# Performance work log

Hardware: AMD Instinct MI355X
Metric: run time of the kernel (lower is better)

## Reference

```python
import jax, jax.numpy as jnp
from jax import lax
import numpy as np

STRIDE = 4
RADIUS = 0.2
NSAMPLE = 32
DENSITY_K = 16
INTRINSIC_DIM = 3
EPS = 1e-8
BN_EPS = 1e-5


def _cdist(a, b):
    # Euclidean pairwise distances: a (..., M, 3), b (..., N, 3) -> (..., M, N)
    d2 = ((a * a).sum(-1)[..., :, None] + (b * b).sum(-1)[..., None, :]
          - 2.0 * jnp.matmul(a, jnp.swapaxes(b, -1, -2)))
    return jnp.sqrt(jnp.maximum(d2, 1e-12))


def _fps(coords, n_samples):
    # iterative farthest point sampling: coords (B, N, 3) -> (B, n_samples) int32
    B, N, _ = coords.shape
    mean = coords.mean(axis=1, keepdims=True)
    farthest = jnp.argmax(((coords - mean) ** 2).sum(-1), axis=1)
    min_dist = jnp.full((B, N), jnp.inf, dtype=coords.dtype)

    def step(carry, _):
        md, far = carry
        centroid = jnp.take_along_axis(coords, far[:, None, None], axis=1)  # (B,1,3)
        d = ((coords - centroid) ** 2).sum(-1)
        md = jnp.minimum(md, d)
        return (md, jnp.argmax(md, axis=1)), far

    _, idxs = lax.scan(step, (min_dist, farthest), None, length=n_samples)
    return idxs.T  # (B, n_samples)


def _ball_query(q, s, radius, k):
    d = _cdist(q, s)  # (B, M, N)
    _, knn_idx = lax.top_k(-d, k)                 # k nearest fallback
    masked = jnp.where(d > radius, jnp.inf, d)
    neg_vals, m_idx = lax.top_k(-masked, k)       # k nearest within radius
    valid = jnp.isfinite(neg_vals)
    return jnp.where(valid, m_idx, knn_idx)


def _density_weights(gc):
    # gc: (B, M, K, 3) -> weights (B, M, K); kth-NN-distance based density weights
    K = gc.shape[2]
    d = _cdist(gc, gc)  # (B, M, K, K)
    d = jnp.where(jnp.eye(K, dtype=bool), jnp.inf, d)
    kk = min(max(DENSITY_K, 1), K - 1)
    kth = -lax.top_k(-d, kk)[0][..., -1]  # distance to kk-th neighbor, (B, M, K)
    raw = jnp.maximum(kth, EPS) ** INTRINSIC_DIM
    return raw / jnp.maximum(raw.sum(axis=-1, keepdims=True), EPS)


def _bn(x, g, b, axes):
    # training-mode batchnorm (biased variance), channel axis = 1
    mu = x.mean(axes, keepdims=True)
    var = x.var(axes, keepdims=True)
    shp = [1] * x.ndim
    shp[1] = -1
    return (x - mu) / jnp.sqrt(var + BN_EPS) * g.reshape(shp) + b.reshape(shp)


def setup_inputs() -> dict:
    key = jax.random.key(0)
    ks = jax.random.split(key, 5)
    B, N, C_in, C_out = 8, 4096, 64, 128
    mid = C_out // 2  # stride > 1 -> mid_channels = out_channels // 2
    coords = jax.random.uniform(ks[0], (B, N, 3), dtype=jnp.float32)
    feats = jax.random.normal(ks[1], (B, C_in, N), dtype=jnp.float32)
    W0 = jax.random.normal(ks[2], (mid, C_in + 3), dtype=jnp.float32) * 0.05
    W1 = jax.random.normal(ks[3], (C_out, mid), dtype=jnp.float32) * 0.05
    Ws = jax.random.normal(ks[4], (C_out, C_in), dtype=jnp.float32) * 0.05
    return {
        "coords": coords, "feats": feats,
        "W0": W0, "g0": jnp.ones((mid,), jnp.float32), "b0": jnp.zeros((mid,), jnp.float32),
        "W1": W1, "g1": jnp.ones((C_out,), jnp.float32), "b1": jnp.zeros((C_out,), jnp.float32),
        "Ws": Ws, "gs": jnp.ones((C_out,), jnp.float32), "bs": jnp.zeros((C_out,), jnp.float32),
    }


def reference(coords, feats, W0, g0, b0, W1, g1, b1, Ws, gs, bs):
    B, N, _ = coords.shape
    M = max(N // STRIDE, 1)
    sample_idx = _fps(coords, M)                               # (B, M)
    gather_pts = jax.vmap(lambda c, i: c[i])                   # (N,3)[idx]
    gather_fts = jax.vmap(lambda f, i: f[:, i])                # (C,N)[:,idx]
    sampled_coords = gather_pts(coords, sample_idx)            # (B, M, 3)
    gidx = _ball_query(sampled_coords, coords, RADIUS, NSAMPLE)  # (B, M, K)
    grouped_coords = gather_pts(coords, gidx)                  # (B, M, K, 3)
    rel = (grouped_coords - sampled_coords[:, :, None, :]) / max(RADIUS, 1e-8)
    grouped_feats = gather_fts(feats, gidx)                    # (B, C_in, M, K)
    x = jnp.concatenate([rel.transpose(0, 3, 1, 2), grouped_feats], axis=1)
    h = jax.nn.relu(_bn(jnp.einsum('oc,bcmk->bomk', W0, x), g0, b0, (0, 2, 3)))
    messages = jax.nn.relu(_bn(jnp.einsum('oc,bcmk->bomk', W1, h), g1, b1, (0, 2, 3)))
    weights = _density_weights(grouped_coords)                 # (B, M, K)
    reduced = (messages * weights[:, None, :, :]).sum(-1)      # (B, C_out, M)
    skip_in = gather_fts(feats, sample_idx)                    # (B, C_in, M)
    skip = _bn(jnp.einsum('oc,bcm->bom', Ws, skip_in), gs, bs, (0, 2))
    return sampled_coords, jax.nn.relu(reduced + skip)
```

## Files before the change

kernel.cpp:

```cpp
#include <hip/hip_runtime.h>
#include <hip/hip_bf16.h>
#include <cstdint>

#define DEV __device__ __forceinline__

constexpr int Bn   = 8;
constexpr int Nn   = 4096;
constexpr int Mn   = 1024;
constexpr int Kn   = 32;
constexpr int CIN  = 64;
constexpr int COUT = 128;

DEV float wave_max_f32(float x) {
#if __has_builtin(__builtin_amdgcn_update_dpp)
#define FSTEP(CTRL, RMASK)                                                      \
  {                                                                             \
    int o = __builtin_amdgcn_update_dpp(0, __float_as_int(x), CTRL, RMASK, 0xf, \
                                        false);                                 \
    x = fmaxf(x, __int_as_float(o));                                            \
  }
  FSTEP(0x111, 0xf)
  FSTEP(0x112, 0xf)
  FSTEP(0x114, 0xf)
  FSTEP(0x118, 0xf)
  FSTEP(0x142, 0xa)
  FSTEP(0x143, 0xc)
#undef FSTEP
#else
  for (int off = 1; off < 64; off <<= 1) x = fmaxf(x, __shfl_xor(x, off, 64));
#endif
  return x;
}

DEV unsigned long long grp8_max_u64(unsigned long long k) {
#if __has_builtin(__builtin_amdgcn_update_dpp)
#define USTEP(CTRL)                                                                    \
  {                                                                                    \
    unsigned int lo = (unsigned int)__builtin_amdgcn_update_dpp(                       \
        0, (int)(unsigned int)k, CTRL, 0xf, 0xf, false);                               \
    unsigned int hi = (unsigned int)__builtin_amdgcn_update_dpp(                       \
        0, (int)(unsigned int)(k >> 32), CTRL, 0xf, 0xf, false);                       \
    unsigned long long o = ((unsigned long long)hi << 32) | lo;                        \
    if (o > k) k = o;                                                                  \
  }
  USTEP(0x111)
  USTEP(0x112)
  USTEP(0x114)
#undef USTEP
#else
  for (int off = 1; off < 8; off <<= 1) {
    unsigned int lo = __shfl_xor((unsigned int)k, off, 64);
    unsigned int hi = __shfl_xor((unsigned int)(k >> 32), off, 64);
    unsigned long long o = ((unsigned long long)hi << 32) | lo;
    if (o > k) k = o;
  }
#endif
  return k;
}

DEV uint32_t fps_round8(const float v[8], int t, unsigned long long (*part)[8], int p) {
  float v4[4]; int j4[4];
#pragma unroll
  for (int i = 0; i < 4; ++i) {
    bool r = v[2 * i + 1] > v[2 * i];
    v4[i] = r ? v[2 * i + 1] : v[2 * i];
    j4[i] = r ? 2 * i + 1 : 2 * i;
  }
  float v2[2]; int j2[2];
#pragma unroll
  for (int i = 0; i < 2; ++i) {
    bool r = v4[2 * i + 1] > v4[2 * i];
    v2[i] = r ? v4[2 * i + 1] : v4[2 * i];
    j2[i] = r ? j4[2 * i + 1] : j4[2 * i];
  }
  bool rr = v2[1] > v2[0];
  float bv = rr ? v2[1] : v2[0];
  int bj = rr ? j2[1] : j2[0];

  float wl = wave_max_f32(bv);
  float wmax = __int_as_float(__builtin_amdgcn_readlane(__float_as_int(wl), 63));
  unsigned long long mask = __ballot(bv == wmax);
  int Ls = (int)__ffsll(mask) - 1;
  int bjw = __shfl(bj, Ls, 64);
  uint32_t idx = 8u * (uint32_t)((t & ~63) + Ls) + (uint32_t)bjw;
  const int sl = p & 1;
  if ((t & 63) == 0)
    part[sl][t >> 6] = ((unsigned long long)__float_as_uint(wmax) << 12) |
                       (unsigned long long)(4095u - idx);
  __syncthreads();
  unsigned long long kk = part[sl][t & 7];
  kk = grp8_max_u64(kk);
  unsigned int lo = (unsigned int)__builtin_amdgcn_readlane((int)(unsigned int)kk, 7);
  return 4095u - (lo & 4095u);
}

__global__ __launch_bounds__(512, 1) void k_fused(const float* __restrict__ coords,
                                                  const float* __restrict__ feats,
                                                  float* __restrict__ featsT,
                                                  uint32_t* __restrict__ sidx,
                                                  float* __restrict__ outc) {
  __shared__ __align__(16) char smraw[Nn * 16];
  __shared__ unsigned long long part[2][8];
  __shared__ uint32_t farl[Mn];
  __shared__ float s_mean[4];
  const int t = threadIdx.x;

  if (blockIdx.x >= 8) {
    float (*tile)[65] = (float(*)[65])smraw;
    int bid = blockIdx.x - 8;
    int b = bid >> 6, n0 = (bid & 63) * 64;
    int lane = t & 63, grp = t >> 6;
    for (int r = 0; r < 8; ++r) {
      int c = grp + r * 8;
      tile[c][lane] = feats[((size_t)b * 64 + c) * 4096 + n0 + lane];
    }
    __syncthreads();
    for (int r = 0; r < 8; ++r) {
      int n = grp + r * 8;
      featsT[((size_t)b * 4096 + n0 + n) * 64 + lane] = tile[lane][n];
    }
    return;
  }

  float4* sp = (float4*)smraw;
  const int b = blockIdx.x;
  const float* cb = coords + (size_t)b * Nn * 3;
  for (int i = t; i < Nn; i += 512)
    sp[i] = make_float4(cb[3 * i], cb[3 * i + 1], cb[3 * i + 2], 0.f);
  __syncthreads();
  if (t == 0) {
    float ax = 0.f, ay = 0.f, az = 0.f;
    for (int i = 0; i < Nn; ++i) {
      float4 c = sp[i];
      ax = __fadd_rn(ax, c.x); ay = __fadd_rn(ay, c.y); az = __fadd_rn(az, c.z);
    }
    s_mean[0] = __fdiv_rn(ax, 4096.f);
    s_mean[1] = __fdiv_rn(ay, 4096.f);
    s_mean[2] = __fdiv_rn(az, 4096.f);
  }
  __syncthreads();

  float px[8], py[8], pz[8], md[8];
#pragma unroll
  for (int j = 0; j < 8; ++j) {
    float4 c = sp[8 * t + j];
    px[j] = c.x; py[j] = c.y; pz[j] = c.z;
    md[j] = __builtin_inff();
  }

  uint32_t far;
  {
    float mx = s_mean[0], my = s_mean[1], mz = s_mean[2];
    float tv[8];
#pragma unroll
    for (int j = 0; j < 8; ++j) {
      float dx = __fsub_rn(px[j], mx), dy = __fsub_rn(py[j], my), dz = __fsub_rn(pz[j], mz);
      tv[j] = __fadd_rn(__fadd_rn(__fmul_rn(dx, dx), __fmul_rn(dy, dy)), __fmul_rn(dz, dz));
    }
    far = fps_round8(tv, t, part, 0);
  }

  for (int p = 1; p < Mn; ++p) {
    if (t == 0) farl[p - 1] = far;
    float4 c = sp[far];
#pragma unroll
    for (int j = 0; j < 8; ++j) {
      float dx = __fsub_rn(px[j], c.x), dy = __fsub_rn(py[j], c.y), dz = __fsub_rn(pz[j], c.z);
      float d = __fadd_rn(__fadd_rn(__fmul_rn(dx, dx), __fmul_rn(dy, dy)), __fmul_rn(dz, dz));
      md[j] = fminf(md[j], d);
    }
    far = fps_round8(md, t, part, p);
  }
  if (t == 0) farl[Mn - 1] = far;
  __syncthreads();

  for (int i = t; i < Mn; i += 512) {
    uint32_t f = farl[i];
    sidx[b * Mn + i] = f;
    float4 c = sp[f];
    outc[(size_t)(b * Mn + i) * 3 + 0] = c.x;
    outc[(size_t)(b * Mn + i) * 3 + 1] = c.y;
    outc[(size_t)(b * Mn + i) * 3 + 2] = c.z;
  }
}

__global__ __launch_bounds__(256) void k_knn(const float* __restrict__ coords,
                                             const uint32_t* __restrict__ sidx,
                                             uint32_t* __restrict__ gidx,
                                             float* __restrict__ wts) {
  const int q = blockIdx.x;
  const int b = q >> 10;
  const int t = threadIdx.x;
  __shared__ unsigned long long keys[Nn + 2];
  __shared__ int s_cnt;
  __shared__ float s_q[4];
  __shared__ uint32_t s_sel[32];
  __shared__ float gx[32], gy[32], gz[32], g2[32];
  __shared__ float dmat[32 * 33];
  __shared__ float kth[32];
  __shared__ float s_raw[32];
  __shared__ float s_sum;

  if (t == 0) {
    uint32_t si = sidx[q];
    const float* c = &coords[((size_t)b * Nn + si) * 3];
    s_q[0] = c[0]; s_q[1] = c[1]; s_q[2] = c[2];
  }
  __syncthreads();
  float qx = s_q[0], qy = s_q[1], qz = s_q[2];
  float q2 = __fadd_rn(__fadd_rn(__fmul_rn(qx, qx), __fmul_rn(qy, qy)), __fmul_rn(qz, qz));
  const float* cb = coords + (size_t)b * Nn * 3;

  float thr = 0.04f;
  int cnt = 0;
  while (true) {
    if (t == 0) s_cnt = 0;
    __syncthreads();
    for (int j = 0; j < 16; ++j) {
      int i = t + 256 * j;
      float cx = cb[3 * i], cy = cb[3 * i + 1], cz = cb[3 * i + 2];
      float c2  = __fadd_rn(__fadd_rn(__fmul_rn(cx, cx), __fmul_rn(cy, cy)), __fmul_rn(cz, cz));
      float dot = __fadd_rn(__fadd_rn(__fmul_rn(qx, cx), __fmul_rn(qy, cy)), __fmul_rn(qz, cz));
      float d2  = __fsub_rn(__fadd_rn(q2, c2), __fmul_rn(2.f, dot));
      float d2c = fmaxf(d2, 1e-12f);
      bool pred = (d2c <= thr);
      unsigned long long mk = __ballot(pred);
      int base = 0;
      if ((t & 63) == 0 && mk) base = atomicAdd(&s_cnt, (int)__popcll(mk));
      base = __shfl(base, 0, 64);
      if (pred) {
        int pos = base + (int)__popcll(mk & ((1ull << (t & 63)) - 1ull));
        keys[pos] = ((unsigned long long)__float_as_uint(d2c) << 32) | (uint32_t)i;
      }
    }
    __syncthreads();
    cnt = s_cnt;
    if (cnt >= 32 || thr > 1.f) break;
    thr = (thr < 0.1f) ? 0.16f : 8.f;
    __syncthreads();
  }
  if (t == 0) { keys[cnt] = ~0ull; keys[cnt + 1] = ~0ull; }
  __syncthreads();
  int cnt2 = (cnt + 1) & ~1;
  for (int i = t; i < cnt; i += 256) {
    unsigned long long ki = keys[i];
    int r = 0;
    for (int j2 = 0; j2 < cnt2; j2 += 2) {
      unsigned long long a = keys[j2], c2 = keys[j2 + 1];
      r += (a < ki) + (c2 < ki);
    }
    if (r < 32) s_sel[r] = (uint32_t)ki;
  }
  __syncthreads();

  if (t < 32) {
    uint32_t gi = s_sel[t];
    gidx[(size_t)q * 32 + t] = gi;
    const float* c = &coords[((size_t)b * Nn + gi) * 3];
    float x = c[0], y = c[1], z = c[2];
    gx[t] = x; gy[t] = y; gz[t] = z;
    g2[t] = __fadd_rn(__fadd_rn(__fmul_rn(x, x), __fmul_rn(y, y)), __fmul_rn(z, z));
  }
  __syncthreads();
  for (int p = t; p < 1024; p += 256) {
    int i = p >> 5, jj = p & 31;
    float dot = __fadd_rn(__fadd_rn(__fmul_rn(gx[i], gx[jj]), __fmul_rn(gy[i], gy[jj])),
                          __fmul_rn(gz[i], gz[jj]));
    float d2 = __fsub_rn(__fadd_rn(g2[i], g2[jj]), __fmul_rn(2.f, dot));
    float dd = sqrtf(fmaxf(d2, 1e-12f));
    if (i == jj) dd = __builtin_inff();
    dmat[i * 33 + jj] = dd;
  }
  __syncthreads();
  for (int p = t; p < 1024; p += 256) {
    int i = p >> 5, jj = p & 31;
    float v = dmat[i * 33 + jj];
    int r = 0;
    for (int c = 0; c < 32; ++c) {
      float u = dmat[i * 33 + c];
      r += (u < v) || (u == v && c < jj);
    }
    if (r == 15) kth[i] = v;
  }
  __syncthreads();
  if (t < 32) { float x = fmaxf(kth[t], 1e-8f); s_raw[t] = x * x * x; }
  __syncthreads();
  if (t == 0) {
    float s = 0.f;
    for (int i2 = 0; i2 < 32; ++i2) s += s_raw[i2];
    s_sum = fmaxf(s, 1e-8f);
  }
  __syncthreads();
  if (t < 32) wts[(size_t)q * 32 + t] = s_raw[t] / s_sum;
}

constexpr int XST = 132;
constexpr int WST = 68;

DEV void build_x(const float* __restrict__ coords, const float* __restrict__ featsT,
                 const uint32_t* __restrict__ sidx, const uint32_t* __restrict__ gidx,
                 const float* __restrict__ W0, int b, int m0, int t,
                 float* xs, float* w0sT, uint32_t* s_gi, float* s_qc) {
  for (int i = t; i < 64 * 67; i += 256) {
    int o = i / 67, c = i - o * 67;
    w0sT[c * WST + o] = W0[i];
  }
  if (t < 128) {
    s_gi[t] = gidx[((size_t)(b * Mn + m0)) * 32 + t];
  } else if (t < 132) {
    int mm = t - 128;
    uint32_t si = sidx[b * Mn + m0 + mm];
    const float* c = &coords[((size_t)b * Nn + si) * 3];
    s_qc[mm * 3 + 0] = c[0]; s_qc[mm * 3 + 1] = c[1]; s_qc[mm * 3 + 2] = c[2];
  }
  __syncthreads();
  if (t < 128) {
    int mm = t >> 5;
    const float* c = &coords[((size_t)b * Nn + s_gi[t]) * 3];
    xs[0 * XST + t] = (c[0] - s_qc[mm * 3 + 0]) / 0.2f;
    xs[1 * XST + t] = (c[1] - s_qc[mm * 3 + 1]) / 0.2f;
    xs[2 * XST + t] = (c[2] - s_qc[mm * 3 + 2]) / 0.2f;
  }
  {
    int c = t & 63, k0g = t >> 6;
    for (int r2 = 0; r2 < 32; ++r2) {
      int kk = k0g + 4 * r2;
      xs[(size_t)(3 + c) * XST + kk] = featsT[((size_t)b * Nn + s_gi[kk]) * 64 + c];
    }
  }
  __syncthreads();
}

DEV void conv1_acc(const float* xs, const float* w0sT, int o0, int k0, float acc[32]) {
#pragma unroll
  for (int i = 0; i < 32; ++i) acc[i] = 0.f;
  for (int c = 0; c < 67; ++c) {
    float4 w  = *(const float4*)&w0sT[c * WST + o0];
    float4 xa = *(const float4*)&xs[c * XST + k0];
    float4 xb = *(const float4*)&xs[c * XST + k0 + 4];
    float wv[4] = {w.x, w.y, w.z, w.w};
    float xv[8] = {xa.x, xa.y, xa.z, xa.w, xb.x, xb.y, xb.z, xb.w};
#pragma unroll
    for (int i = 0; i < 4; ++i)
#pragma unroll
      for (int j = 0; j < 8; ++j)
        acc[i * 8 + j] = fmaf(wv[i], xv[j], acc[i * 8 + j]);
  }
}

DEV void conv2_acc(const float* hs, const float* w1sT, int o0, int k0, float acc2[32]) {
#pragma unroll
  for (int i = 0; i < 32; ++i) acc2[i] = 0.f;
  for (int c = 0; c < 64; ++c) {
    float4 w  = *(const float4*)&w1sT[c * WST + o0];
    float4 xa = *(const float4*)&hs[c * XST + k0];
    float4 xb = *(const float4*)&hs[c * XST + k0 + 4];
    float wv[4] = {w.x, w.y, w.z, w.w};
    float xv[8] = {xa.x, xa.y, xa.z, xa.w, xb.x, xb.y, xb.z, xb.w};
#pragma unroll
    for (int i = 0; i < 4; ++i)
#pragma unroll
      for (int j = 0; j < 8; ++j)
        acc2[i * 8 + j] = fmaf(wv[i], xv[j], acc2[i * 8 + j]);
  }
}

__global__ __launch_bounds__(256) void k_conv1(const float* __restrict__ coords,
                                               const float* __restrict__ featsT,
                                               const uint32_t* __restrict__ sidx,
                                               const uint32_t* __restrict__ gidx,
                                               const float* __restrict__ W0,
                                               float* __restrict__ stats,
                                               unsigned short* __restrict__ accb) {
  __shared__ float xs[67 * XST];
  __shared__ float w0sT[67 * WST];
  __shared__ uint32_t s_gi[128];
  __shared__ float s_qc[12];
  __shared__ float ssum[64], ssq[64];
  int blk = blockIdx.x, t = threadIdx.x;
  int b = blk >> 8, m0 = (blk & 255) << 2;
  if (t < 64) { ssum[t] = 0.f; ssq[t] = 0.f; }
  build_x(coords, featsT, sidx, gidx, W0, b, m0, t, xs, w0sT, s_gi, s_qc);
  int o0 = (t & 15) * 4, k0 = (t >> 4) * 8;
  float acc[32];
  conv1_acc(xs, w0sT, o0, k0, acc);
  if (accb != nullptr) {
    unsigned short* at = accb + (size_t)blk * 8192;
#pragma unroll
    for (int i = 0; i < 4; ++i) {
      unsigned int w[4];
#pragma unroll
      for (int q = 0; q < 4; ++q) {
        __hip_bfloat16 h0 = __float2bfloat16(acc[i * 8 + 2 * q]);
        __hip_bfloat16 h1 = __float2bfloat16(acc[i * 8 + 2 * q + 1]);
        unsigned short u0 = *reinterpret_cast<unsigned short*>(&h0);
        unsigned short u1 = *reinterpret_cast<unsigned short*>(&h1);
        w[q] = (unsigned int)u0 | ((unsigned int)u1 << 16);
      }
      uint4 v = make_uint4(w[0], w[1], w[2], w[3]);
      *(uint4*)&at[(o0 + i) * 128 + k0] = v;
    }
  }
#pragma unroll
  for (int i = 0; i < 4; ++i) {
    float s = 0.f, sq = 0.f;
#pragma unroll
    for (int j = 0; j < 8; ++j) { s += acc[i * 8 + j]; sq = fmaf(acc[i * 8 + j], acc[i * 8 + j], sq); }
    atomicAdd(&ssum[o0 + i], s); atomicAdd(&ssq[o0 + i], sq);
  }
  __syncthreads();
  if (t < 64) { atomicAdd(&stats[t], ssum[t]); atomicAdd(&stats[64 + t], ssq[t]); }
}

__global__ __launch_bounds__(256) void k_conv2c(const unsigned short* __restrict__ accb,
                                                const float* __restrict__ W1,
                                                float* __restrict__ stats,
                                                const float* __restrict__ g0,
                                                const float* __restrict__ b0) {
  __shared__ float hs[64 * XST];
  __shared__ float w1sT[64 * WST];
  __shared__ float s_a0[64], s_c0[64];
  __shared__ float ssum[128], ssq[128];
  int blk = blockIdx.x, t = threadIdx.x;
  if (t < 128) { ssum[t] = 0.f; ssq[t] = 0.f; }
  if (t < 64) {
    float mu  = stats[t] * (1.f / 262144.f);
    float var = stats[64 + t] * (1.f / 262144.f) - mu * mu;
    float a = g0[t] / sqrtf(var + 1e-5f);
    s_a0[t] = a; s_c0[t] = b0[t] - mu * a;
  }
  const unsigned short* at = accb + (size_t)blk * 8192;
  int o = t >> 2, kb = (t & 3) * 32;
  __syncthreads();
  float a0 = s_a0[o], c0 = s_c0[o];
#pragma unroll
  for (int g = 0; g < 4; ++g) {
    uint4 v = *(const uint4*)&at[o * 128 + kb + 8 * g];
    unsigned int vv[4] = {v.x, v.y, v.z, v.w};
#pragma unroll
    for (int q = 0; q < 4; ++q) {
      float f0 = __uint_as_float((vv[q] & 0xffffu) << 16);
      float f1 = __uint_as_float(vv[q] & 0xffff0000u);
      hs[o * XST + kb + 8 * g + 2 * q]     = fmaxf(fmaf(a0, f0, c0), 0.f);
      hs[o * XST + kb + 8 * g + 2 * q + 1] = fmaxf(fmaf(a0, f1, c0), 0.f);
    }
  }
  int o0 = (t & 15) * 4, k0 = (t >> 4) * 8;
  for (int p = 0; p < 2; ++p) {
    __syncthreads();
    for (int i = t; i < 64 * 64; i += 256) {
      int oo = i >> 6, cc = i & 63;
      w1sT[cc * WST + oo] = W1[(size_t)(64 * p + oo) * 64 + cc];
    }
    __syncthreads();
    float acc2[32];
    conv2_acc(hs, w1sT, o0, k0, acc2);
#pragma unroll
    for (int i = 0; i < 4; ++i) {
      float s = 0.f, sq = 0.f;
#pragma unroll
      for (int j = 0; j < 8; ++j) { s += acc2[i * 8 + j]; sq = fmaf(acc2[i * 8 + j], acc2[i * 8 + j], sq); }
      atomicAdd(&ssum[64 * p + o0 + i], s); atomicAdd(&ssq[64 * p + o0 + i], sq);
    }
  }
  __syncthreads();
  if (t < 128) { atomicAdd(&stats[128 + t], ssum[t]); atomicAdd(&stats[256 + t], ssq[t]); }
}

__global__ __launch_bounds__(256) void k_outc(const unsigned short* __restrict__ accb,
                                              const float* __restrict__ W1,
                                              const float* __restrict__ wts,
                                              const float* __restrict__ ys,
                                              const float* __restrict__ stats,
                                              const float* __restrict__ g0,
                                              const float* __restrict__ b0,
                                              const float* __restrict__ g1,
                                              const float* __restrict__ b1,
                                              const float* __restrict__ gs,
                                              const float* __restrict__ bs,
                                              float* __restrict__ out_feat) {
  __shared__ float hs[64 * XST];
  __shared__ float w1sT[64 * WST];
  __shared__ float s_a0[64], s_c0[64];
  __shared__ float s_a1[128], s_c1[128], s_as[128], s_cs[128];
  __shared__ __align__(16) float sw[4 * 36];
  __shared__ float red[128 * 5];
  int blk = blockIdx.x, t = threadIdx.x;
  int b = blk >> 8, m0 = (blk & 255) << 2;
  if (t < 64) {
    float mu  = stats[t] * (1.f / 262144.f);
    float var = stats[64 + t] * (1.f / 262144.f) - mu * mu;
    float a = g0[t] / sqrtf(var + 1e-5f);
    s_a0[t] = a; s_c0[t] = b0[t] - mu * a;
  }
  if (t < 128) {
    float mu  = stats[128 + t] * (1.f / 262144.f);
    float var = stats[256 + t] * (1.f / 262144.f) - mu * mu;
    float a = g1[t] / sqrtf(var + 1e-5f);
    s_a1[t] = a; s_c1[t] = b1[t] - mu * a;
    float mus  = stats[384 + t] * (1.f / 8192.f);
    float vars = stats[512 + t] * (1.f / 8192.f) - mus * mus;
    float as = gs[t] / sqrtf(vars + 1e-5f);
    s_as[t] = as; s_cs[t] = bs[t] - mus * as;
    sw[(t >> 5) * 36 + (t & 31)] = wts[((size_t)(b * Mn + m0)) * 32 + t];
  }
  const unsigned short* at = accb + (size_t)blk * 8192;
  int o = t >> 2, kb = (t & 3) * 32;
  __syncthreads();
  float a0 = s_a0[o], c0 = s_c0[o];
#pragma unroll
  for (int g = 0; g < 4; ++g) {
    uint4 v = *(const uint4*)&at[o * 128 + kb + 8 * g];
    unsigned int vv[4] = {v.x, v.y, v.z, v.w};
#pragma unroll
    for (int q = 0; q < 4; ++q) {
      float f0 = __uint_as_float((vv[q] & 0xffffu) << 16);
      float f1 = __uint_as_float(vv[q] & 0xffff0000u);
      hs[o * XST + kb + 8 * g + 2 * q]     = fmaxf(fmaf(a0, f0, c0), 0.f);
      hs[o * XST + kb + 8 * g + 2 * q + 1] = fmaxf(fmaf(a0, f1, c0), 0.f);
    }
  }
  int o0 = (t & 15) * 4, k0 = (t >> 4) * 8;
  int m = k0 >> 5, nb0 = k0 & 31;
  for (int p = 0; p < 2; ++p) {
    __syncthreads();
    for (int i = t; i < 64 * 64; i += 256) {
      int oo = i >> 6, cc = i & 63;
      w1sT[cc * WST + oo] = W1[(size_t)(64 * p + oo) * 64 + cc];
    }
    __syncthreads();
    float acc2[32];
    conv2_acc(hs, w1sT, o0, k0, acc2);
    float4 swa = *(const float4*)&sw[m * 36 + nb0];
    float4 swb = *(const float4*)&sw[m * 36 + nb0 + 4];
    float wv[8] = {swa.x, swa.y, swa.z, swa.w, swb.x, swb.y, swb.z, swb.w};
    float a1v[4], c1v[4];
#pragma unroll
    for (int i = 0; i < 4; ++i) { a1v[i] = s_a1[64 * p + o0 + i]; c1v[i] = s_c1[64 * p + o0 + i]; }
    float r4[4];
#pragma unroll
    for (int i = 0; i < 4; ++i) {
      float r = 0.f;
#pragma unroll
      for (int j = 0; j < 8; ++j) {
        float msg = fmaxf(fmaf(a1v[i], acc2[i * 8 + j], c1v[i]), 0.f);
        r = fmaf(msg, wv[j], r);
      }
      r4[i] = r;
    }
#pragma unroll
    for (int i = 0; i < 4; ++i) {
      float r = r4[i];
      r += __shfl_xor(r, 16, 64);
      r += __shfl_xor(r, 32, 64);
      r4[i] = r;
    }
    if ((t & 63) < 16) {
      float4 ysv = *(const float4*)&ys[((size_t)(b * Mn + m0 + m)) * 128 + 64 * p + o0];
      float yv[4] = {ysv.x, ysv.y, ysv.z, ysv.w};
#pragma unroll
      for (int i = 0; i < 4; ++i) {
        int o2 = 64 * p + o0 + i;
        red[o2 * 5 + m] = fmaxf(r4[i] + fmaf(s_as[o2], yv[i], s_cs[o2]), 0.f);
      }
    }
  }
  __syncthreads();
  for (int e = t; e < 512; e += 256) {
    int oo = e >> 2, mm = e & 3;
    out_feat[(size_t)b * 131072 + (size_t)oo * 1024 + m0 + mm] = red[oo * 5 + mm];
  }
}

__global__ void k_fin0(float* stats, const float* g0, const float* b0) {
  int t = threadIdx.x;
  if (t >= 64) return;
  float mu  = stats[t] * (1.f / 262144.f);
  float var = stats[64 + t] * (1.f / 262144.f) - mu * mu;
  float a = g0[t] / sqrtf(var + 1e-5f);
  stats[640 + t] = a;
  stats[704 + t] = b0[t] - mu * a;
}

__global__ __launch_bounds__(256) void k_conv2(const float* __restrict__ coords,
                                               const float* __restrict__ featsT,
                                               const uint32_t* __restrict__ sidx,
                                               const uint32_t* __restrict__ gidx,
                                               const float* __restrict__ W0,
                                               const float* __restrict__ W1,
                                               float* __restrict__ stats) {
  __shared__ float smU[13400];
  __shared__ uint32_t s_gi[128];
  __shared__ float s_qc[12];
  __shared__ float ssum[128], ssq[128];
  float* xs = smU;  float* w0sT = smU + 67 * XST;
  float* hs = smU;  float* w1sT = smU + 64 * XST;
  int blk = blockIdx.x, t = threadIdx.x;
  int b = blk >> 8, m0 = (blk & 255) << 2;
  if (t < 128) { ssum[t] = 0.f; ssq[t] = 0.f; }
  build_x(coords, featsT, sidx, gidx, W0, b, m0, t, xs, w0sT, s_gi, s_qc);
  int o0 = (t & 15) * 4, k0 = (t >> 4) * 8;
  float acc[32];
  conv1_acc(xs, w0sT, o0, k0, acc);
  float4 a04 = *(const float4*)&stats[640 + o0];
  float4 c04 = *(const float4*)&stats[704 + o0];
  float a0v[4] = {a04.x, a04.y, a04.z, a04.w};
  float c0v[4] = {c04.x, c04.y, c04.z, c04.w};
  __syncthreads();
#pragma unroll
  for (int i = 0; i < 4; ++i) {
    float h[8];
#pragma unroll
    for (int j = 0; j < 8; ++j) h[j] = fmaxf(fmaf(a0v[i], acc[i * 8 + j], c0v[i]), 0.f);
    *(float4*)&hs[(o0 + i) * XST + k0]     = make_float4(h[0], h[1], h[2], h[3]);
    *(float4*)&hs[(o0 + i) * XST + k0 + 4] = make_float4(h[4], h[5], h[6], h[7]);
  }
  for (int p = 0; p < 2; ++p) {
    __syncthreads();
    for (int i = t; i < 64 * 64; i += 256) {
      int oo = i >> 6, cc = i & 63;
      w1sT[cc * WST + oo] = W1[(size_t)(64 * p + oo) * 64 + cc];
    }
    __syncthreads();
    float acc2[32];
    conv2_acc(hs, w1sT, o0, k0, acc2);
#pragma unroll
    for (int i = 0; i < 4; ++i) {
      float s = 0.f, sq = 0.f;
#pragma unroll
      for (int j = 0; j < 8; ++j) { s += acc2[i * 8 + j]; sq = fmaf(acc2[i * 8 + j], acc2[i * 8 + j], sq); }
      atomicAdd(&ssum[64 * p + o0 + i], s); atomicAdd(&ssq[64 * p + o0 + i], sq);
    }
  }
  __syncthreads();
  if (t < 128) { atomicAdd(&stats[128 + t], ssum[t]); atomicAdd(&stats[256 + t], ssq[t]); }
}

__global__ __launch_bounds__(256) void k_skip(const float* __restrict__ featsT,
                                              const uint32_t* __restrict__ sidx,
                                              const float* __restrict__ Ws,
                                              float* __restrict__ ys,
                                              float* __restrict__ stats) {
  __shared__ float fin[64 * 65];
  __shared__ float wssT[64 * 129];
  __shared__ uint32_t s_si[64];
  __shared__ float ssum[128], ssq[128];
  int blk = blockIdx.x, t = threadIdx.x;
  int b = blk >> 4, m0 = (blk & 15) * 64;
  if (t < 64) s_si[t] = sidx[b * Mn + m0 + t];
  if (t < 128) { ssum[t] = 0.f; ssq[t] = 0.f; }
  __syncthreads();
  for (int i = t; i < 64 * 64; i += 256) {
    int mm = i >> 6, c = i & 63;
    fin[mm * 65 + c] = featsT[((size_t)b * Nn + s_si[mm]) * 64 + c];
  }
  for (int i = t; i < 128 * 64; i += 256) {
    int oo = i >> 6, cc = i & 63;
    wssT[cc * 129 + oo] = Ws[(size_t)oo * 64 + cc];
  }
  __syncthreads();
  int o = t & 127, mh = t >> 7;
  float s = 0.f, sq = 0.f;
  for (int mm = mh * 32; mm < mh * 32 + 32; ++mm) {
    float acc = 0.f;
    for (int c = 0; c < 64; ++c) acc = fmaf(wssT[c * 129 + o], fin[mm * 65 + c], acc);
    ys[((size_t)(b * Mn + m0 + mm)) * 128 + o] = acc;
    s += acc; sq = fmaf(acc, acc, sq);
  }
  atomicAdd(&ssum[o], s); atomicAdd(&ssq[o], sq);
  __syncthreads();
  if (t < 128) { atomicAdd(&stats[384 + t], ssum[t]); atomicAdd(&stats[512 + t], ssq[t]); }
}

__global__ void k_fin1(float* stats, const float* g1, const float* b1,
                       const float* gs, const float* bs) {
  int t = threadIdx.x;
  if (t >= 128) return;
  float mu  = stats[128 + t] * (1.f / 262144.f);
  float var = stats[256 + t] * (1.f / 262144.f) - mu * mu;
  float a = g1[t] / sqrtf(var + 1e-5f);
  stats[768 + t] = a;
  stats[896 + t] = b1[t] - mu * a;
  float mus  = stats[384 + t] * (1.f / 8192.f);
  float vars = stats[512 + t] * (1.f / 8192.f) - mus * mus;
  float as = gs[t] / sqrtf(vars + 1e-5f);
  stats[1024 + t] = as;
  stats[1152 + t] = bs[t] - mus * as;
}

__global__ __launch_bounds__(256) void k_out(const float* __restrict__ coords,
                                             const float* __restrict__ featsT,
                                             const uint32_t* __restrict__ sidx,
                                             const uint32_t* __restrict__ gidx,
                                             const float* __restrict__ W0,
                                             const float* __restrict__ W1,
                                             const float* __restrict__ wts,
                                             const float* __restrict__ ys,
                                             const float* __restrict__ stats,
                                             float* __restrict__ out_feat) {
  __shared__ float smU[13400];
  __shared__ uint32_t s_gi[128];
  __shared__ float s_qc[12];
  __shared__ __align__(16) float sw[4 * 36];
  __shared__ float red[128 * 5];
  float* xs = smU;  float* w0sT = smU + 67 * XST;
  float* hs = smU;  float* w1sT = smU + 64 * XST;
  int blk = blockIdx.x, t = threadIdx.x;
  int b = blk >> 8, m0 = (blk & 255) << 2;
  build_x(coords, featsT, sidx, gidx, W0, b, m0, t, xs, w0sT, s_gi, s_qc);
  if (t < 128) sw[(t >> 5) * 36 + (t & 31)] = wts[((size_t)(b * Mn + m0)) * 32 + t];
  int o0 = (t & 15) * 4, k0 = (t >> 4) * 8;
  int m = k0 >> 5, nb0 = k0 & 31;
  float acc[32];
  conv1_acc(xs, w0sT, o0, k0, acc);
  float4 a04 = *(const float4*)&stats[640 + o0];
  float4 c04 = *(const float4*)&stats[704 + o0];
  float a0v[4] = {a04.x, a04.y, a04.z, a04.w};
  float c0v[4] = {c04.x, c04.y, c04.z, c04.w};
  __syncthreads();
#pragma unroll
  for (int i = 0; i < 4; ++i) {
    float h[8];
#pragma unroll
    for (int j = 0; j < 8; ++j) h[j] = fmaxf(fmaf(a0v[i], acc[i * 8 + j], c0v[i]), 0.f);
    *(float4*)&hs[(o0 + i) * XST + k0]     = make_float4(h[0], h[1], h[2], h[3]);
    *(float4*)&hs[(o0 + i) * XST + k0 + 4] = make_float4(h[4], h[5], h[6], h[7]);
  }
  for (int p = 0; p < 2; ++p) {
    __syncthreads();
    for (int i = t; i < 64 * 64; i += 256) {
      int oo = i >> 6, cc = i & 63;
      w1sT[cc * WST + oo] = W1[(size_t)(64 * p + oo) * 64 + cc];
    }
    __syncthreads();
    float acc2[32];
    conv2_acc(hs, w1sT, o0, k0, acc2);
    float4 swa = *(const float4*)&sw[m * 36 + nb0];
    float4 swb = *(const float4*)&sw[m * 36 + nb0 + 4];
    float wv[8] = {swa.x, swa.y, swa.z, swa.w, swb.x, swb.y, swb.z, swb.w};
    float4 a14 = *(const float4*)&stats[768 + 64 * p + o0];
    float4 c14 = *(const float4*)&stats[896 + 64 * p + o0];
    float a1v[4] = {a14.x, a14.y, a14.z, a14.w};
    float c1v[4] = {c14.x, c14.y, c14.z, c14.w};
    float r4[4];
#pragma unroll
    for (int i = 0; i < 4; ++i) {
      float r = 0.f;
#pragma unroll
      for (int j = 0; j < 8; ++j) {
        float msg = fmaxf(fmaf(a1v[i], acc2[i * 8 + j], c1v[i]), 0.f);
        r = fmaf(msg, wv[j], r);
      }
      r4[i] = r;
    }
#pragma unroll
    for (int i = 0; i < 4; ++i) {
      float r = r4[i];
      r += __shfl_xor(r, 16, 64);
      r += __shfl_xor(r, 32, 64);
      r4[i] = r;
    }
    if ((t & 63) < 16) {
      float4 ysv = *(const float4*)&ys[((size_t)(b * Mn + m0 + m)) * 128 + 64 * p + o0];
      float4 as4 = *(const float4*)&stats[1024 + 64 * p + o0];
      float4 cs4 = *(const float4*)&stats[1152 + 64 * p + o0];
      float yv[4] = {ysv.x, ysv.y, ysv.z, ysv.w};
      float av[4] = {as4.x, as4.y, as4.z, as4.w};
      float cv[4] = {cs4.x, cs4.y, cs4.z, cs4.w};
#pragma unroll
      for (int i = 0; i < 4; ++i)
        red[(64 * p + o0 + i) * 5 + m] = fmaxf(r4[i] + fmaf(av[i], yv[i], cv[i]), 0.f);
    }
  }
  __syncthreads();
  for (int e = t; e < 512; e += 256) {
    int oo = e >> 2, mm = e & 3;
    out_feat[(size_t)b * 131072 + (size_t)oo * 1024 + m0 + mm] = red[oo * 5 + mm];
  }
}

extern "C" void kernel_launch(void* const* d_in, const int* in_sizes, int n_in,
                              void* d_out, int out_size, void* d_ws, size_t ws_size,
                              hipStream_t stream) {
  const float* coords = (const float*)d_in[0];
  const float* feats  = (const float*)d_in[1];
  const float* W0 = (const float*)d_in[2];
  const float* g0 = (const float*)d_in[3];
  const float* b0 = (const float*)d_in[4];
  const float* W1 = (const float*)d_in[5];
  const float* g1 = (const float*)d_in[6];
  const float* b1 = (const float*)d_in[7];
  const float* Ws = (const float*)d_in[8];
  const float* gs = (const float*)d_in[9];
  const float* bs = (const float*)d_in[10];

  float* out_coords = (float*)d_out;
  float* out_feat   = out_coords + (size_t)Bn * Mn * 3;

  char* w = (char*)d_ws;
  float*    featsT = (float*)w;    w += (size_t)Bn * Nn * CIN * 4;
  uint32_t* sidx   = (uint32_t*)w; w += (size_t)Bn * Mn * 4;
  uint32_t* gidx   = (uint32_t*)w; w += (size_t)Bn * Mn * Kn * 4;
  float*    wts    = (float*)w;    w += (size_t)Bn * Mn * Kn * 4;
  float*    ys     = (float*)w;    w += (size_t)Bn * Mn * COUT * 4;
  unsigned short* accb = (unsigned short*)w; w += (size_t)2048 * 8192 * 2;
  float*    stats  = (float*)w;    w += 1280 * 4;
  const bool cachemode = ws_size >= (size_t)(w - (char*)d_ws);

  hipMemsetAsync(stats, 0, 640 * 4, stream);
  hipLaunchKernelGGL(k_fused, dim3(520),  dim3(512), 0, stream,
                     coords, feats, featsT, sidx, out_coords);
  hipLaunchKernelGGL(k_knn,   dim3(8192), dim3(256), 0, stream, coords, sidx, gidx, wts);
  hipLaunchKernelGGL(k_conv1, dim3(2048), dim3(256), 0, stream,
                     coords, featsT, sidx, gidx, W0, stats,
                     cachemode ? accb : (unsigned short*)nullptr);
  hipLaunchKernelGGL(k_skip,  dim3(128),  dim3(256), 0, stream, featsT, sidx, Ws, ys, stats);
  if (cachemode) {
    hipLaunchKernelGGL(k_conv2c, dim3(2048), dim3(256), 0, stream, accb, W1, stats, g0, b0);
    hipLaunchKernelGGL(k_outc,   dim3(2048), dim3(256), 0, stream,
                       accb, W1, wts, ys, stats, g0, b0, g1, b1, gs, bs, out_feat);
  } else {
    hipLaunchKernelGGL(k_fin0,  dim3(1),    dim3(64),  0, stream, stats, g0, b0);
    hipLaunchKernelGGL(k_conv2, dim3(2048), dim3(256), 0, stream,
                       coords, featsT, sidx, gidx, W0, W1, stats);
    hipLaunchKernelGGL(k_fin1,  dim3(1),    dim3(128), 0, stream, stats, g1, b1, gs, bs);
    hipLaunchKernelGGL(k_out,   dim3(2048), dim3(256), 0, stream,
                       coords, featsT, sidx, gidx, W0, W1, wts, ys, stats, out_feat);
  }
}
```

Measured before the change: 1.100 ms.

## Cache conv2 output in bf16, merge skip conv into conv1 launch

Adds a new workspace tier that stores the second-layer conv outputs as bf16 in k_conv2c, so the final kernel (k_outc2) only applies BN, ReLU, the density weighting and the skip path instead of recomputing conv2. The skip projection kernel is folded into the conv1 launch as extra blocks to drop a launch and overlap with conv1. The FPS argmax also swaps a lane shuffle for ballot-based reconstruction of the index. This adds a large extra workspace buffer and depends on ws_size being big enough for the new path to run.

```diff
diff --git a/kernel.cpp b/kernel.cpp
--- a/kernel.cpp
+++ b/kernel.cpp
@@ -77,11 +77,15 @@
   float bv = rr ? v2[1] : v2[0];
   int bj = rr ? j2[1] : j2[0];
 
+  unsigned long long mb0 = __ballot((bj & 1) != 0);
+  unsigned long long mb1 = __ballot((bj & 2) != 0);
+  unsigned long long mb2 = __ballot((bj & 4) != 0);
   float wl = wave_max_f32(bv);
   float wmax = __int_as_float(__builtin_amdgcn_readlane(__float_as_int(wl), 63));
   unsigned long long mask = __ballot(bv == wmax);
   int Ls = (int)__ffsll(mask) - 1;
-  int bjw = __shfl(bj, Ls, 64);
+  int bjw = (int)((mb0 >> Ls) & 1ull) | ((int)((mb1 >> Ls) & 1ull) << 1) |
+            ((int)((mb2 >> Ls) & 1ull) << 2);
   uint32_t idx = 8u * (uint32_t)((t & ~63) + Ls) + (uint32_t)bjw;
   const int sl = p & 1;
   if ((t & 63) == 0)
@@ -365,19 +369,61 @@
   }
 }
 
-__global__ __launch_bounds__(256) void k_conv1(const float* __restrict__ coords,
-                                               const float* __restrict__ featsT,
-                                               const uint32_t* __restrict__ sidx,
-                                               const uint32_t* __restrict__ gidx,
-                                               const float* __restrict__ W0,
-                                               float* __restrict__ stats,
-                                               unsigned short* __restrict__ accb) {
-  __shared__ float xs[67 * XST];
-  __shared__ float w0sT[67 * WST];
+DEV unsigned short f2bf(float x) {
+  __hip_bfloat16 h = __float2bfloat16(x);
+  return *reinterpret_cast<unsigned short*>(&h);
+}
+
+
+__global__ __launch_bounds__(256) void k_conv1s(const float* __restrict__ coords,
+                                                const float* __restrict__ featsT,
+                                                const uint32_t* __restrict__ sidx,
+                                                const uint32_t* __restrict__ gidx,
+                                                const float* __restrict__ W0,
+                                                const float* __restrict__ Ws,
+                                                float* __restrict__ ys,
+                                                float* __restrict__ stats,
+                                                unsigned short* __restrict__ accb) {
+  __shared__ float smU[13400];
   __shared__ uint32_t s_gi[128];
   __shared__ float s_qc[12];
-  __shared__ float ssum[64], ssq[64];
-  int blk = blockIdx.x, t = threadIdx.x;
+  __shared__ float ssum[128], ssq[128];
+  int t = threadIdx.x;
+
+  if (blockIdx.x >= 2048) {
+    float* fin  = smU;
+    float* wssT = smU + 64 * 65;
+    uint32_t* s_si = s_gi;
+    int blk = blockIdx.x - 2048;
+    int b = blk >> 4, m0 = (blk & 15) * 64;
+    if (t < 64) s_si[t] = sidx[b * Mn + m0 + t];
+    if (t < 128) { ssum[t] = 0.f; ssq[t] = 0.f; }
+    __syncthreads();
+    for (int i = t; i < 64 * 64; i += 256) {
+      int mm = i >> 6, c = i & 63;
+      fin[mm * 65 + c] = featsT[((size_t)b * Nn + s_si[mm]) * 64 + c];
+    }
+    for (int i = t; i < 128 * 64; i += 256) {
+      int oo = i >> 6, cc = i & 63;
+      wssT[cc * 129 + oo] = Ws[(size_t)oo * 64 + cc];
+    }
+    __syncthreads();
+    int o = t & 127, mh = t >> 7;
+    float s = 0.f, sq = 0.f;
+    for (int mm = mh * 32; mm < mh * 32 + 32; ++mm) {
+      float acc = 0.f;
+      for (int c = 0; c < 64; ++c) acc = fmaf(wssT[c * 129 + o], fin[mm * 65 + c], acc);
+      ys[((size_t)(b * Mn + m0 + mm)) * 128 + o] = acc;
+      s += acc; sq = fmaf(acc, acc, sq);
+    }
+    atomicAdd(&ssum[o], s); atomicAdd(&ssq[o], sq);
+    __syncthreads();
+    if (t < 128) { atomicAdd(&stats[384 + t], ssum[t]); atomicAdd(&stats[512 + t], ssq[t]); }
+    return;
+  }
+
+  float* xs = smU; float* w0sT = smU + 67 * XST;
+  int blk = blockIdx.x;
   int b = blk >> 8, m0 = (blk & 255) << 2;
   if (t < 64) { ssum[t] = 0.f; ssq[t] = 0.f; }
   build_x(coords, featsT, sidx, gidx, W0, b, m0, t, xs, w0sT, s_gi, s_qc);
@@ -390,15 +436,10 @@
     for (int i = 0; i < 4; ++i) {
       unsigned int w[4];
 #pragma unroll
-      for (int q = 0; q < 4; ++q) {
-        __hip_bfloat16 h0 = __float2bfloat16(acc[i * 8 + 2 * q]);
-        __hip_bfloat16 h1 = __float2bfloat16(acc[i * 8 + 2 * q + 1]);
-        unsigned short u0 = *reinterpret_cast<unsigned short*>(&h0);
-        unsigned short u1 = *reinterpret_cast<unsigned short*>(&h1);
-        w[q] = (unsigned int)u0 | ((unsigned int)u1 << 16);
-      }
-      uint4 v = make_uint4(w[0], w[1], w[2], w[3]);
-      *(uint4*)&at[(o0 + i) * 128 + k0] = v;
+      for (int q = 0; q < 4; ++q)
+        w[q] = (unsigned int)f2bf(acc[i * 8 + 2 * q]) |
+               ((unsigned int)f2bf(acc[i * 8 + 2 * q + 1]) << 16);
+      *(uint4*)&at[(o0 + i) * 128 + k0] = make_uint4(w[0], w[1], w[2], w[3]);
     }
   }
 #pragma unroll
@@ -416,7 +457,8 @@
                                                 const float* __restrict__ W1,
                                                 float* __restrict__ stats,
                                                 const float* __restrict__ g0,
-                                                const float* __restrict__ b0) {
+                                                const float* __restrict__ b0,
+                                                unsigned short* __restrict__ acc2b) {
   __shared__ float hs[64 * XST];
   __shared__ float w1sT[64 * WST];
   __shared__ float s_a0[64], s_c0[64];
@@ -446,6 +488,7 @@
     }
   }
   int o0 = (t & 15) * 4, k0 = (t >> 4) * 8;
+  unsigned short* at2 = (acc2b != nullptr) ? acc2b + (size_t)blk * 16384 : nullptr;
   for (int p = 0; p < 2; ++p) {
     __syncthreads();
     for (int i = t; i < 64 * 64; i += 256) {
@@ -455,6 +498,16 @@
     __syncthreads();
     float acc2[32];
     conv2_acc(hs, w1sT, o0, k0, acc2);
+    if (at2 != nullptr) {
+#pragma unroll
+      for (int j = 0; j < 8; ++j) {
+        unsigned int lo = (unsigned int)f2bf(acc2[0 * 8 + j]) |
+                          ((unsigned int)f2bf(acc2[1 * 8 + j]) << 16);
+        unsigned int hi = (unsigned int)f2bf(acc2[2 * 8 + j]) |
+                          ((unsigned int)f2bf(acc2[3 * 8 + j]) << 16);
+        *(uint2*)&at2[(size_t)(k0 + j) * 128 + 64 * p + o0] = make_uint2(lo, hi);
+      }
+    }
 #pragma unroll
     for (int i = 0; i < 4; ++i) {
       float s = 0.f, sq = 0.f;
@@ -465,6 +518,57 @@
   }
   __syncthreads();
   if (t < 128) { atomicAdd(&stats[128 + t], ssum[t]); atomicAdd(&stats[256 + t], ssq[t]); }
+}
+
+__global__ __launch_bounds__(256) void k_outc2(const unsigned short* __restrict__ acc2b,
+                                               const float* __restrict__ wts,
+                                               const float* __restrict__ ys,
+                                               const float* __restrict__ stats,
+                                               const float* __restrict__ g1,
+                                               const float* __restrict__ b1,
+                                               const float* __restrict__ gs,
+                                               const float* __restrict__ bs,
+                                               float* __restrict__ out_feat) {
+  __shared__ float s_a1[128], s_c1[128], s_as[128], s_cs[128];
+  __shared__ float sw[4 * 36];
+  __shared__ float red[128 * 5];
+  int blk = blockIdx.x, t = threadIdx.x;
+  int b = blk >> 8, m0 = (blk & 255) << 2;
+  if (t < 128) {
+    float mu  = stats[128 + t] * (1.f / 262144.f);
+    float var = stats[256 + t] * (1.f / 262144.f) - mu * mu;
+    float a = g1[t] / sqrtf(var + 1e-5f);
+    s_a1[t] = a; s_c1[t] = b1[t] - mu * a;
+    float mus  = stats[384 + t] * (1.f / 8192.f);
+    float vars = stats[512 + t] * (1.f / 8192.f) - mus * mus;
+    float as = gs[t] / sqrtf(vars + 1e-5f);
+    s_as[t] = as; s_cs[t] = bs[t] - mus * as;
+    sw[(t >> 5) * 36 + (t & 31)] = wts[((size_t)(b * Mn + m0)) * 32 + t];
+  }
+  __syncthreads();
+  int o2 = t & 127, mh = t >> 7;
+  float a1 = s_a1[o2], c1 = s_c1[o2], as = s_as[o2], cs = s_cs[o2];
+  const unsigned short* base = acc2b + (size_t)blk * 16384;
+#pragma unroll
+  for (int mi = 0; mi < 2; ++mi) {
+    int m = mh * 2 + mi;
+    const unsigned short* col = base + (size_t)(m * 32) * 128 + o2;
+    const float* swr = &sw[m * 36];
+    float r = 0.f;
+#pragma unroll
+    for (int k = 0; k < 32; ++k) {
+      float f = __uint_as_float((unsigned int)col[(size_t)k * 128] << 16);
+      float msg = fmaxf(fmaf(a1, f, c1), 0.f);
+      r = fmaf(msg, swr[k], r);
+    }
+    float ysv = ys[((size_t)(b * Mn + m0 + m)) * 128 + o2];
+    red[o2 * 5 + m] = fmaxf(r + fmaf(as, ysv, cs), 0.f);
+  }
+  __syncthreads();
+  for (int e = t; e < 512; e += 256) {
+    int oo = e >> 2, mm = e & 3;
+    out_feat[(size_t)b * 131072 + (size_t)oo * 1024 + m0 + mm] = red[oo * 5 + mm];
+  }
 }
 
 __global__ __launch_bounds__(256) void k_outc(const unsigned short* __restrict__ accb,
@@ -634,42 +738,6 @@
   }
   __syncthreads();
   if (t < 128) { atomicAdd(&stats[128 + t], ssum[t]); atomicAdd(&stats[256 + t], ssq[t]); }
-}
-
-__global__ __launch_bounds__(256) void k_skip(const float* __restrict__ featsT,
-                                              const uint32_t* __restrict__ sidx,
-                                              const float* __restrict__ Ws,
-                                              float* __restrict__ ys,
-                                              float* __restrict__ stats) {
-  __shared__ float fin[64 * 65];
-  __shared__ float wssT[64 * 129];
-  __shared__ uint32_t s_si[64];
-  __shared__ float ssum[128], ssq[128];
-  int blk = blockIdx.x, t = threadIdx.x;
-  int b = blk >> 4, m0 = (blk & 15) * 64;
-  if (t < 64) s_si[t] = sidx[b * Mn + m0 + t];
-  if (t < 128) { ssum[t] = 0.f; ssq[t] = 0.f; }
-  __syncthreads();
-  for (int i = t; i < 64 * 64; i += 256) {
-    int mm = i >> 6, c = i & 63;
-    fin[mm * 65 + c] = featsT[((size_t)b * Nn + s_si[mm]) * 64 + c];
-  }
-  for (int i = t; i < 128 * 64; i += 256) {
-    int oo = i >> 6, cc = i & 63;
-    wssT[cc * 129 + oo] = Ws[(size_t)oo * 64 + cc];
-  }
-  __syncthreads();
-  int o = t & 127, mh = t >> 7;
-  float s = 0.f, sq = 0.f;
-  for (int mm = mh * 32; mm < mh * 32 + 32; ++mm) {
-    float acc = 0.f;
-    for (int c = 0; c < 64; ++c) acc = fmaf(wssT[c * 129 + o], fin[mm * 65 + c], acc);
-    ys[((size_t)(b * Mn + m0 + mm)) * 128 + o] = acc;
-    s += acc; sq = fmaf(acc, acc, sq);
-  }
-  atomicAdd(&ssum[o], s); atomicAdd(&ssq[o], sq);
-  __syncthreads();
-  if (t < 128) { atomicAdd(&stats[384 + t], ssum[t]); atomicAdd(&stats[512 + t], ssq[t]); }
 }
 
 __global__ void k_fin1(float* stats, const float* g1, const float* b1,
@@ -805,18 +873,27 @@
   float*    ys     = (float*)w;    w += (size_t)Bn * Mn * COUT * 4;
   unsigned short* accb = (unsigned short*)w; w += (size_t)2048 * 8192 * 2;
   float*    stats  = (float*)w;    w += 1280 * 4;
-  const bool cachemode = ws_size >= (size_t)(w - (char*)d_ws);
+  size_t needB = (size_t)(w - (char*)d_ws);
+  unsigned short* acc2b = (unsigned short*)w; w += (size_t)2048 * 16384 * 2;
+  size_t needA = (size_t)(w - (char*)d_ws);
+  const bool tierA = ws_size >= needA;
+  const bool tierB = ws_size >= needB;
 
   hipMemsetAsync(stats, 0, 640 * 4, stream);
   hipLaunchKernelGGL(k_fused, dim3(520),  dim3(512), 0, stream,
                      coords, feats, featsT, sidx, out_coords);
   hipLaunchKernelGGL(k_knn,   dim3(8192), dim3(256), 0, stream, coords, sidx, gidx, wts);
-  hipLaunchKernelGGL(k_conv1, dim3(2048), dim3(256), 0, stream,
-                     coords, featsT, sidx, gidx, W0, stats,
-                     cachemode ? accb : (unsigned short*)nullptr);
-  hipLaunchKernelGGL(k_skip,  dim3(128),  dim3(256), 0, stream, featsT, sidx, Ws, ys, stats);
-  if (cachemode) {
-    hipLaunchKernelGGL(k_conv2c, dim3(2048), dim3(256), 0, stream, accb, W1, stats, g0, b0);
+  hipLaunchKernelGGL(k_conv1s, dim3(2176), dim3(256), 0, stream,
+                     coords, featsT, sidx, gidx, W0, Ws, ys, stats,
+                     tierB ? accb : (unsigned short*)nullptr);
+  if (tierA) {
+    hipLaunchKernelGGL(k_conv2c, dim3(2048), dim3(256), 0, stream,
+                       accb, W1, stats, g0, b0, acc2b);
+    hipLaunchKernelGGL(k_outc2,  dim3(2048), dim3(256), 0, stream,
+                       acc2b, wts, ys, stats, g1, b1, gs, bs, out_feat);
+  } else if (tierB) {
+    hipLaunchKernelGGL(k_conv2c, dim3(2048), dim3(256), 0, stream,
+                       accb, W1, stats, g0, b0, (unsigned short*)nullptr);
     hipLaunchKernelGGL(k_outc,   dim3(2048), dim3(256), 0, stream,
                        accb, W1, wts, ys, stats, g0, b0, g1, b1, gs, bs, out_feat);
   } else {
```

After: 1.045 ms. 5.0% less time.
